# Kernel tuning notes

Measured on AMD Instinct MI355X. Metric: run time of the kernel, lower is better.

The kernel has to match this reference:

```python
import math
import jax, jax.numpy as jnp
import numpy as np

B, S, HID = 2, 1024, 2048
H, D, R = 16, 128, 64            # heads, head_dim, rope_dim_per_head
KVC, QC = 512, 1536              # kv / query compressed dims
MAX_POS = 4096


def _lin(x, w, b):
    return x @ w.T + b


def _rotate_half(x):
    x1, x2 = x[..., : x.shape[-1] // 2], x[..., x.shape[-1] // 2 :]
    return jnp.concatenate([-x2, x1], axis=-1)


def _rope_tables(dim, end, theta=10000.0):
    freqs = 1.0 / (theta ** (jnp.arange(0, dim, 2)[: dim // 2].astype(jnp.float32) / dim))
    f = jnp.outer(jnp.arange(end, dtype=jnp.float32), freqs)  # [end, dim//2]
    cos, sin = jnp.cos(f), jnp.sin(f)
    # duplicate halves so tables broadcast against the full rope dim (standard HF convention)
    return jnp.concatenate([cos, cos], -1), jnp.concatenate([sin, sin], -1)


def setup_inputs() -> dict:
    key = jax.random.key(0)
    ks = jax.random.split(key, 17)
    w = lambda k, shape: (jax.random.normal(k, shape, jnp.float32) * 0.02)
    return {
        "hidden_states": jax.random.normal(ks[0], (B, S, HID), jnp.float32),
        "W_DKV_w": w(ks[1], (KVC, HID)),  "W_DKV_b": w(ks[2], (KVC,)),
        "W_UK_w":  w(ks[3], (H * D, KVC)), "W_UK_b":  w(ks[4], (H * D,)),
        "W_UV_w":  w(ks[5], (H * D, KVC)), "W_UV_b":  w(ks[6], (H * D,)),
        "W_KR_w":  w(ks[7], (R, D)),       "W_KR_b":  w(ks[8], (R,)),
        "W_DQ_w":  w(ks[9], (QC, HID)),    "W_DQ_b":  w(ks[10], (QC,)),
        "W_UQ_w":  w(ks[11], (H * D, QC)), "W_UQ_b":  w(ks[12], (H * D,)),
        "W_QR_w":  w(ks[13], (R, D)),      "W_QR_b":  w(ks[14], (R,)),
        "W_O_w":   w(ks[15], (HID, H * D)),"W_O_b":   w(ks[16], (HID,)),
    }


def reference(hidden_states, W_DKV_w, W_DKV_b, W_UK_w, W_UK_b, W_UV_w, W_UV_b,
              W_KR_w, W_KR_b, W_DQ_w, W_DQ_b, W_UQ_w, W_UQ_b,
              W_QR_w, W_QR_b, W_O_w, W_O_b):
    b, s = hidden_states.shape[:2]
    # latent KV compression + decompression
    c_kv = _lin(hidden_states, W_DKV_w, W_DKV_b)                      # [B,S,KVC]
    k = _lin(c_kv, W_UK_w, W_UK_b).reshape(b, s, H, D)
    v = _lin(c_kv, W_UV_w, W_UV_b).reshape(b, s, H, D)
    # latent Q compression + decompression
    c_q = _lin(hidden_states, W_DQ_w, W_DQ_b)                         # [B,S,QC]
    q = _lin(c_q, W_UQ_w, W_UQ_b).reshape(b, s, H, D)
    # decoupled rope sub-dims
    k_r = _lin(k, W_KR_w, W_KR_b)                                     # [B,S,H,R]
    q_r = _lin(q, W_QR_w, W_QR_b)                                     # [B,S,H,R]
    cos, sin = _rope_tables(R, MAX_POS)
    cos_p = cos[:s][:, None, :]                                       # [S,1,R] -> broadcast over B,H
    sin_p = sin[:s][:, None, :]
    q_r = q_r * cos_p + _rotate_half(q_r) * sin_p
    k_r = k_r * cos_p + _rotate_half(k_r) * sin_p
    # SDPA (no mask, no causal flag in original)
    scale = 1.0 / math.sqrt(D)
    scores = jnp.einsum("bqhd,bkhd->bhqk", q, k) * scale              # [B,H,S,S]
    probs = jax.nn.softmax(scores, axis=-1)
    attn = jnp.einsum("bhqk,bkhd->bqhd", probs, v).reshape(b, s, H * D)
    output = _lin(attn, W_O_w, W_O_b)                                 # [B,S,HID]
    return output, c_kv, k_r
```

## Files before the change

### kernel.cpp

```cpp
#include <hip/hip_runtime.h>
#include <cstdint>

typedef __bf16 bf16;
typedef __attribute__((ext_vector_type(8))) __bf16 bf16x8;
typedef __attribute__((ext_vector_type(4))) float f32x4;

#define MFMA16(a, b, c) __builtin_amdgcn_mfma_f32_16x16x32_bf16(a, b, c, 0, 0, 0)

__device__ __forceinline__ void async16(const bf16* g, bf16* l) {
  __builtin_amdgcn_global_load_lds(
      (const __attribute__((address_space(1))) void*)g,
      (__attribute__((address_space(3))) void*)l, 16, 0, 0);
}

__device__ __forceinline__ bf16x8 load8cvt(const float* p) {
  f32x4 a = *(const f32x4*)p;
  f32x4 b = *(const f32x4*)(p + 4);
  bf16x8 r;
  r[0] = (bf16)a[0]; r[1] = (bf16)a[1]; r[2] = (bf16)a[2]; r[3] = (bf16)a[3];
  r[4] = (bf16)b[0]; r[5] = (bf16)b[1]; r[6] = (bf16)b[2]; r[7] = (bf16)b[3];
  return r;
}

__global__ __launch_bounds__(256) void cvt_f32_bf16(const float* __restrict__ src,
                                                    bf16* __restrict__ dst, int n) {
  int i = (blockIdx.x * 256 + threadIdx.x) * 8;
  if (i >= n) return;
  *(bf16x8*)(dst + i) = load8cvt(src + i);
}

__global__ __launch_bounds__(256) void cvt6(
    const float* __restrict__ s0, bf16* __restrict__ d0, int n0,
    const float* __restrict__ s1, bf16* __restrict__ d1, int n1,
    const float* __restrict__ s2, bf16* __restrict__ d2, int n2,
    const float* __restrict__ s3, bf16* __restrict__ d3, int n3,
    const float* __restrict__ s4, bf16* __restrict__ d4, int n4,
    const float* __restrict__ s5, bf16* __restrict__ d5, int n5) {
  const float* s; bf16* d; int n;
  switch (blockIdx.y) {
    case 0: s = s0; d = d0; n = n0; break;
    case 1: s = s1; d = d1; n = n1; break;
    case 2: s = s2; d = d2; n = n2; break;
    case 3: s = s3; d = d3; n = n3; break;
    case 4: s = s4; d = d4; n = n4; break;
    default: s = s5; d = d5; n = n5; break;
  }
  int i = (blockIdx.x * 256 + threadIdx.x) * 8;
  if (i >= n) return;
  *(bf16x8*)(d + i) = load8cvt(s + i);
}

template <int MODE>
__global__ __launch_bounds__(256) void gemm_bb(
    const bf16* __restrict__ A, int lda,
    const bf16* __restrict__ Bm, int ldb,
    const float* __restrict__ bias0, const float* __restrict__ bias1, int nsplit,
    bf16* __restrict__ outb, float* __restrict__ outf, int ldo,
    int M, int N, int K) {
  __shared__ __align__(16) bf16 As[2][128 * 32];
  __shared__ __align__(16) bf16 Bs[2][64 * 32];
  const int t = threadIdx.x;
  const int lane = t & 63, w = t >> 6;
  const int quad = lane >> 4, l15 = lane & 15;

  const int nwg = gridDim.x * gridDim.y;
  const int id = blockIdx.y * gridDim.x + blockIdx.x;
  const int sw = (id & 7) * (nwg >> 3) + (id >> 3);
  const int bm = (sw / gridDim.x) * 128, bn = (sw % gridDim.x) * 64;

  const int wm = (w >> 1) * 64, wn = (w & 1) * 32;

  f32x4 acc[4][2] = {};

  const int srow = t >> 2;
  const int scol = (t & 3) * 8;
  const bf16* Ap = A + (int64_t)(bm + srow) * lda + scol;
  const bf16* Bp = Bm + (int64_t)(bn + srow) * ldb + scol;

  auto STAGE = [&](int buf, int k0) {
    async16(Ap + k0, &As[buf][w * 512]);
    async16(Ap + (int64_t)64 * lda + k0, &As[buf][2048 + w * 512]);
    async16(Bp + k0, &Bs[buf][w * 512]);
  };
  auto COMPUTE = [&](int buf) {
    bf16x8 a[4], bq[2];
#pragma unroll
    for (int mt = 0; mt < 4; ++mt)
      a[mt] = *(const bf16x8*)(&As[buf][(wm + mt * 16 + l15) * 32 + quad * 8]);
#pragma unroll
    for (int nt = 0; nt < 2; ++nt)
      bq[nt] = *(const bf16x8*)(&Bs[buf][(wn + nt * 16 + l15) * 32 + quad * 8]);
#pragma unroll
    for (int mt = 0; mt < 4; ++mt)
#pragma unroll
      for (int nt = 0; nt < 2; ++nt)
        acc[mt][nt] = MFMA16(a[mt], bq[nt], acc[mt][nt]);
  };

  STAGE(0, 0);
  for (int k0 = 0; k0 < K; k0 += 64) {
    STAGE(1, k0 + 32);
    asm volatile("s_waitcnt vmcnt(3)\n\ts_barrier" ::: "memory");
    COMPUTE(0);
    asm volatile("s_waitcnt lgkmcnt(0)\n\ts_barrier" ::: "memory");
    if (k0 + 64 < K) {
      STAGE(0, k0 + 64);
      asm volatile("s_waitcnt vmcnt(3)\n\ts_barrier" ::: "memory");
    } else {
      asm volatile("s_waitcnt vmcnt(0)\n\ts_barrier" ::: "memory");
    }
    COMPUTE(1);
    asm volatile("s_waitcnt lgkmcnt(0)\n\ts_barrier" ::: "memory");
  }

  float bv[2];
#pragma unroll
  for (int nt = 0; nt < 2; ++nt) {
    int n = bn + wn + nt * 16 + l15;
    bv[nt] = (n < nsplit) ? bias0[n] : bias1[n - nsplit];
  }
#pragma unroll
  for (int mt = 0; mt < 4; ++mt)
#pragma unroll
    for (int nt = 0; nt < 2; ++nt)
#pragma unroll
      for (int r = 0; r < 4; ++r) {
        int64_t m = bm + wm + mt * 16 + quad * 4 + r;
        int n = bn + wn + nt * 16 + l15;
        float v = acc[mt][nt][r] + bv[nt];
        if (MODE != 1) outb[m * ldo + n] = (bf16)v;
        if (MODE == 1) outf[m * (int64_t)ldo + n] = v;
        if (MODE == 2 && n < nsplit) outf[m * nsplit + n] = v;
      }
}

__global__ __launch_bounds__(256) void kr_rope(const bf16* __restrict__ kmat,
                                               const float* __restrict__ Wkr,
                                               const float* __restrict__ bkr,
                                               float* __restrict__ krout) {
  const int t = threadIdx.x;
  const int lane = t & 63, w = t >> 6;
  const int quad = lane >> 4, l15 = lane & 15;
  const int row0 = blockIdx.x * 64 + w * 16;

  const int rr = row0 + l15;
  const bf16* krow = kmat + (int64_t)(rr >> 4) * 4096 + (rr & 15) * 128;
  bf16x8 af[4];
#pragma unroll
  for (int ks = 0; ks < 4; ++ks)
    af[ks] = *(const bf16x8*)(krow + ks * 32 + quad * 8);

  f32x4 acc[4] = {};
#pragma unroll
  for (int nt = 0; nt < 4; ++nt)
#pragma unroll
    for (int ks = 0; ks < 4; ++ks) {
      bf16x8 bf_ = load8cvt(Wkr + (nt * 16 + l15) * 128 + ks * 32 + quad * 8);
      acc[nt] = MFMA16(af[ks], bf_, acc[nt]);
    }

  float bv[4], fr[4];
#pragma unroll
  for (int nt = 0; nt < 4; ++nt) {
    bv[nt] = bkr[nt * 16 + l15];
    int j = ((nt & 1) * 16 + l15);
    fr[nt] = exp2f(-(float)j * 0.41524101186092034f);
  }

#pragma unroll
  for (int r = 0; r < 4; ++r) {
    int row = row0 + quad * 4 + r;
    int pos = (row >> 4) & 1023;
    float val[4];
#pragma unroll
    for (int nt = 0; nt < 4; ++nt) val[nt] = acc[nt][r] + bv[nt];
#pragma unroll
    for (int nt = 0; nt < 4; ++nt) {
      int n = nt * 16 + l15;
      float ang = (float)pos * fr[nt];
      float c = cosf(ang), s = sinf(ang);
      float partner = val[nt ^ 2];
      float o = val[nt] * c + ((nt < 2) ? -partner : partner) * s;
      krout[(int64_t)row * 64 + n] = o;
    }
  }
}

__global__ __launch_bounds__(512, 2) void attn_fwd(const bf16* __restrict__ q,
                                                   const bf16* __restrict__ k,
                                                   const bf16* __restrict__ v,
                                                   bf16* __restrict__ attn) {
  const int bh = blockIdx.x * 4 + (blockIdx.y >> 3);
  const int qt = blockIdx.y & 7;
  const int b = bh >> 4, h = bh & 15;
  __shared__ __align__(16) bf16 Kb[2][64 * 128];
  __shared__ __align__(16) bf16 Vt[128 * 72];
  __shared__ __align__(16) bf16 Pl[8][16 * 72];

  const int t = threadIdx.x;
  const int lane = t & 63, w = t >> 6;
  const int quad = lane >> 4, l15 = lane & 15;
  const int trow = b * 1024 + qt * 128 + w * 16;
  const float scale = 0.08838834764831845f;

  bf16x8 qf[4];
#pragma unroll
  for (int ks = 0; ks < 4; ++ks)
    qf[ks] = *(const bf16x8*)(q + (int64_t)(trow + l15) * 2048 + h * 128 +
                              ks * 32 + quad * 8);

  const bf16* kbase = k + (int64_t)b * 1024 * 4096 + h * 128;
  const int lrow = lane >> 4;
  const int64_t koff0 = (int64_t)(w * 8 + lrow) * 4096 + (((lane & 15) ^ lrow) << 3);
  const int64_t koff1 = (int64_t)(w * 8 + 4 + lrow) * 4096 +
                        (((lane & 15) ^ (4 + lrow)) << 3);

  const int skey = t >> 4;
  const int sd0 = (t & 15) * 8;
  const bf16* vp = v + (int64_t)b * 1024 * 4096 + h * 128 + sd0;

  async16(kbase + koff0, &Kb[0][w * 1024]);
  async16(kbase + koff1, &Kb[0][w * 1024 + 512]);
  bf16x8 vreg[2];
#pragma unroll
  for (int r = 0; r < 2; ++r)
    vreg[r] = *(const bf16x8*)(vp + (int64_t)(r * 32 + skey) * 4096);

  f32x4 o[8] = {};
  float lrw[4] = {0.f, 0.f, 0.f, 0.f};

  for (int kt = 0; kt < 16; ++kt) {
    const int cur = kt & 1;
#pragma unroll
    for (int r = 0; r < 2; ++r) {
      int key = r * 32 + skey;
      int col = (((key >> 3) ^ ((sd0 >> 3) & 7)) << 3) + (key & 7);
#pragma unroll
      for (int j = 0; j < 8; ++j) Vt[(sd0 + j) * 72 + col] = vreg[r][j];
    }
    __syncthreads();

    if (kt + 1 < 16) {
      const bf16* kn = kbase + (int64_t)(kt + 1) * 64 * 4096;
      async16(kn + koff0, &Kb[cur ^ 1][w * 1024]);
      async16(kn + koff1, &Kb[cur ^ 1][w * 1024 + 512]);
#pragma unroll
      for (int r = 0; r < 2; ++r)
        vreg[r] = *(const bf16x8*)(vp + (int64_t)((kt + 1) * 64 + r * 32 + skey) * 4096);
    }

    f32x4 s[4] = {};
    __builtin_amdgcn_s_setprio(1);
#pragma unroll
    for (int nt = 0; nt < 4; ++nt)
#pragma unroll
      for (int ks = 0; ks < 4; ++ks) {
        int key = nt * 16 + l15;
        bf16x8 bfrg = *(const bf16x8*)(
            &Kb[cur][key * 128 + (((ks * 4 + quad) ^ (l15 & 7)) << 3)]);
        s[nt] = MFMA16(qf[ks], bfrg, s[nt]);
      }
    __builtin_amdgcn_s_setprio(0);

    float rsum[4] = {0.f, 0.f, 0.f, 0.f};
#pragma unroll
    for (int nt = 0; nt < 4; ++nt)
#pragma unroll
      for (int r = 0; r < 4; ++r) {
        float p = __expf(s[nt][r] * scale);
        rsum[r] += p;
        int row = quad * 4 + r;
        int blk = (nt * 2 + (l15 >> 3)) ^ (quad * 2 + (r >> 1));
        Pl[w][row * 72 + (blk << 3) + (l15 & 7)] = (bf16)p;
      }
#pragma unroll
    for (int r = 0; r < 4; ++r) lrw[r] += rsum[r];

    __builtin_amdgcn_s_setprio(1);
#pragma unroll
    for (int ks = 0; ks < 2; ++ks) {
      int ablk = (ks * 4 + quad) ^ (l15 >> 1);
      bf16x8 afrg = *(const bf16x8*)(&Pl[w][l15 * 72 + (ablk << 3)]);
#pragma unroll
      for (int dt = 0; dt < 8; ++dt) {
        int d = dt * 16 + l15;
        int kb = ((ks * 4 + quad) ^ ((d >> 3) & 7)) << 3;
        bf16x8 bfrg = *(const bf16x8*)(Vt + d * 72 + kb);
        o[dt] = MFMA16(afrg, bfrg, o[dt]);
      }
    }
    __builtin_amdgcn_s_setprio(0);
    asm volatile("s_waitcnt lgkmcnt(0)\n\ts_barrier" ::: "memory");
  }

  float inv[4];
#pragma unroll
  for (int r = 0; r < 4; ++r) {
    float ssum = lrw[r];
#pragma unroll
    for (int off = 8; off >= 1; off >>= 1) ssum += __shfl_xor(ssum, off, 64);
    inv[r] = 1.0f / ssum;
  }
#pragma unroll
  for (int dt = 0; dt < 8; ++dt)
#pragma unroll
    for (int r = 0; r < 4; ++r) {
      int64_t row = trow + quad * 4 + r;
      int col = h * 128 + dt * 16 + l15;
      attn[row * 2048 + col] = (bf16)(o[dt][r] * inv[r]);
    }
}

extern "C" void kernel_launch(void* const* d_in, const int* in_sizes, int n_in,
                              void* d_out, int out_size, void* d_ws, size_t ws_size,
                              hipStream_t stream) {
  const float* hidden = (const float*)d_in[0];
  const float* Wdkv = (const float*)d_in[1];
  const float* bdkv = (const float*)d_in[2];
  const float* Wuk  = (const float*)d_in[3];
  const float* buk  = (const float*)d_in[4];
  const float* Wuv  = (const float*)d_in[5];
  const float* buv  = (const float*)d_in[6];
  const float* Wkr  = (const float*)d_in[7];
  const float* bkr  = (const float*)d_in[8];
  const float* Wdq  = (const float*)d_in[9];
  const float* bdq  = (const float*)d_in[10];
  const float* Wuq  = (const float*)d_in[11];
  const float* buq  = (const float*)d_in[12];
  const float* Wo   = (const float*)d_in[15];
  const float* bo   = (const float*)d_in[16];

  float* out0 = (float*)d_out;
  float* c_kv = out0 + 4194304;
  float* k_r  = out0 + 5242880;

  bf16* DKVQ = (bf16*)d_ws;
  bf16* KV   = DKVQ + 4194304;

  bf16* WT   = KV;
  bf16* qx   = (bf16*)out0;
  bf16* hb   = qx + 4194304;
  bf16* WUKV = qx;
  bf16* Wuqb = hb;
  bf16* Wob  = (bf16*)k_r;

  cvt6<<<dim3(2048, 6), 256, 0, stream>>>(
      hidden, hb, 4194304,
      Wdkv, WT, 1048576,
      Wdq, WT + 1048576, 3145728,
      Wuk, WUKV, 1048576,
      Wuv, WUKV + 1048576, 1048576,
      Wo, Wob, 4194304);
  gemm_bb<2><<<dim3(32, 16), 256, 0, stream>>>(hb, 2048, WT, 2048, bdkv, bdq, 512,
                                               DKVQ, c_kv, 2048, 2048, 2048, 2048);
  cvt_f32_bf16<<<1536, 256, 0, stream>>>(Wuq, Wuqb, 3145728);
  gemm_bb<0><<<dim3(64, 16), 256, 0, stream>>>(DKVQ, 2048, WUKV, 512, buk, buv, 2048,
                                               KV, nullptr, 4096, 2048, 4096, 512);
  gemm_bb<0><<<dim3(32, 16), 256, 0, stream>>>(DKVQ + 512, 2048, Wuqb, 1536, buq, buq,
                                               2048, qx, nullptr, 2048, 2048, 2048, 1536);
  attn_fwd<<<dim3(8, 32), 512, 0, stream>>>(qx, KV, KV + 2048, DKVQ);
  gemm_bb<1><<<dim3(32, 16), 256, 0, stream>>>(DKVQ, 2048, Wob, 2048, bo, bo, 2048,
                                               nullptr, out0, 2048, 2048, 2048, 2048);
  kr_rope<<<512, 256, 0, stream>>>(KV, Wkr, bkr, k_r);
}
```

Baseline: 312.1 us.

## Deepen GEMM prefetch to four stages and halve attention block size

The GEMM mainloop moves from a two-buffer ping-pong to a four-slot ring buffer with three K-slices in flight, and the vmcnt waits are adjusted so the tail drains correctly. This is meant to hide more global-load latency, at the cost of doubling LDS use per block. The attention kernel drops from 512 to 256 threads per block (64 query rows instead of 128) and uses twice as many blocks, so each thread now loads four K/V rows per tile. This raises block count for better CU fill but means each K/V tile is reloaded by twice as many blocks.

```diff
diff --git a/kernel.cpp b/kernel.cpp
--- a/kernel.cpp
+++ b/kernel.cpp
@@ -57,8 +57,8 @@
     const float* __restrict__ bias0, const float* __restrict__ bias1, int nsplit,
     bf16* __restrict__ outb, float* __restrict__ outf, int ldo,
     int M, int N, int K) {
-  __shared__ __align__(16) bf16 As[2][128 * 32];
-  __shared__ __align__(16) bf16 Bs[2][64 * 32];
+  __shared__ __align__(16) bf16 As[4][128 * 32];
+  __shared__ __align__(16) bf16 Bs[4][64 * 32];
   const int t = threadIdx.x;
   const int lane = t & 63, w = t >> 6;
   const int quad = lane >> 4, l15 = lane & 15;
@@ -97,19 +97,21 @@
         acc[mt][nt] = MFMA16(a[mt], bq[nt], acc[mt][nt]);
   };
 
+  const int K32 = K >> 5;
   STAGE(0, 0);
-  for (int k0 = 0; k0 < K; k0 += 64) {
-    STAGE(1, k0 + 32);
-    asm volatile("s_waitcnt vmcnt(3)\n\ts_barrier" ::: "memory");
-    COMPUTE(0);
-    asm volatile("s_waitcnt lgkmcnt(0)\n\ts_barrier" ::: "memory");
-    if (k0 + 64 < K) {
-      STAGE(0, k0 + 64);
-      asm volatile("s_waitcnt vmcnt(3)\n\ts_barrier" ::: "memory");
+  STAGE(1, 32);
+  STAGE(2, 64);
+  for (int s = 0; s < K32; ++s) {
+    if (s + 3 < K32) {
+      STAGE((s + 3) & 3, (s + 3) << 5);
+      asm volatile("s_waitcnt vmcnt(9)\n\ts_barrier" ::: "memory");
     } else {
-      asm volatile("s_waitcnt vmcnt(0)\n\ts_barrier" ::: "memory");
-    }
-    COMPUTE(1);
+      const int rem = K32 - 1 - s;
+      if (rem >= 2)      asm volatile("s_waitcnt vmcnt(6)\n\ts_barrier" ::: "memory");
+      else if (rem == 1) asm volatile("s_waitcnt vmcnt(3)\n\ts_barrier" ::: "memory");
+      else               asm volatile("s_waitcnt vmcnt(0)\n\ts_barrier" ::: "memory");
+    }
+    COMPUTE(s & 3);
     asm volatile("s_waitcnt lgkmcnt(0)\n\ts_barrier" ::: "memory");
   }
 
@@ -186,21 +188,21 @@
   }
 }
 
-__global__ __launch_bounds__(512, 2) void attn_fwd(const bf16* __restrict__ q,
+__global__ __launch_bounds__(256, 2) void attn_fwd(const bf16* __restrict__ q,
                                                    const bf16* __restrict__ k,
                                                    const bf16* __restrict__ v,
                                                    bf16* __restrict__ attn) {
-  const int bh = blockIdx.x * 4 + (blockIdx.y >> 3);
-  const int qt = blockIdx.y & 7;
+  const int bh = blockIdx.x * 4 + (blockIdx.y >> 4);
+  const int qt = blockIdx.y & 15;
   const int b = bh >> 4, h = bh & 15;
   __shared__ __align__(16) bf16 Kb[2][64 * 128];
   __shared__ __align__(16) bf16 Vt[128 * 72];
-  __shared__ __align__(16) bf16 Pl[8][16 * 72];
+  __shared__ __align__(16) bf16 Pl[4][16 * 72];
 
   const int t = threadIdx.x;
   const int lane = t & 63, w = t >> 6;
   const int quad = lane >> 4, l15 = lane & 15;
-  const int trow = b * 1024 + qt * 128 + w * 16;
+  const int trow = b * 1024 + qt * 64 + w * 16;
   const float scale = 0.08838834764831845f;
 
   bf16x8 qf[4];
@@ -211,20 +213,24 @@
 
   const bf16* kbase = k + (int64_t)b * 1024 * 4096 + h * 128;
   const int lrow = lane >> 4;
-  const int64_t koff0 = (int64_t)(w * 8 + lrow) * 4096 + (((lane & 15) ^ lrow) << 3);
-  const int64_t koff1 = (int64_t)(w * 8 + 4 + lrow) * 4096 +
-                        (((lane & 15) ^ (4 + lrow)) << 3);
+  int64_t koff[4];
+#pragma unroll
+  for (int c = 0; c < 4; ++c) {
+    int row = w * 16 + c * 4 + lrow;
+    koff[c] = (int64_t)row * 4096 + (((lane & 15) ^ (row & 7)) << 3);
+  }
 
   const int skey = t >> 4;
   const int sd0 = (t & 15) * 8;
   const bf16* vp = v + (int64_t)b * 1024 * 4096 + h * 128 + sd0;
 
-  async16(kbase + koff0, &Kb[0][w * 1024]);
-  async16(kbase + koff1, &Kb[0][w * 1024 + 512]);
-  bf16x8 vreg[2];
-#pragma unroll
-  for (int r = 0; r < 2; ++r)
-    vreg[r] = *(const bf16x8*)(vp + (int64_t)(r * 32 + skey) * 4096);
+#pragma unroll
+  for (int c = 0; c < 4; ++c)
+    async16(kbase + koff[c], &Kb[0][w * 2048 + c * 512]);
+  bf16x8 vreg[4];
+#pragma unroll
+  for (int r = 0; r < 4; ++r)
+    vreg[r] = *(const bf16x8*)(vp + (int64_t)(r * 16 + skey) * 4096);
 
   f32x4 o[8] = {};
   float lrw[4] = {0.f, 0.f, 0.f, 0.f};
@@ -232,8 +238,8 @@
   for (int kt = 0; kt < 16; ++kt) {
     const int cur = kt & 1;
 #pragma unroll
-    for (int r = 0; r < 2; ++r) {
-      int key = r * 32 + skey;
+    for (int r = 0; r < 4; ++r) {
+      int key = r * 16 + skey;
       int col = (((key >> 3) ^ ((sd0 >> 3) & 7)) << 3) + (key & 7);
 #pragma unroll
       for (int j = 0; j < 8; ++j) Vt[(sd0 + j) * 72 + col] = vreg[r][j];
@@ -242,11 +248,12 @@
 
     if (kt + 1 < 16) {
       const bf16* kn = kbase + (int64_t)(kt + 1) * 64 * 4096;
-      async16(kn + koff0, &Kb[cur ^ 1][w * 1024]);
-      async16(kn + koff1, &Kb[cur ^ 1][w * 1024 + 512]);
-#pragma unroll
-      for (int r = 0; r < 2; ++r)
-        vreg[r] = *(const bf16x8*)(vp + (int64_t)((kt + 1) * 64 + r * 32 + skey) * 4096);
+#pragma unroll
+      for (int c = 0; c < 4; ++c)
+        async16(kn + koff[c], &Kb[cur ^ 1][w * 2048 + c * 512]);
+#pragma unroll
+      for (int r = 0; r < 4; ++r)
+        vreg[r] = *(const bf16x8*)(vp + (int64_t)((kt + 1) * 64 + r * 16 + skey) * 4096);
     }
 
     f32x4 s[4] = {};
@@ -358,7 +365,7 @@
                                                KV, nullptr, 4096, 2048, 4096, 512);
   gemm_bb<0><<<dim3(32, 16), 256, 0, stream>>>(DKVQ + 512, 2048, Wuqb, 1536, buq, buq,
                                                2048, qx, nullptr, 2048, 2048, 2048, 1536);
-  attn_fwd<<<dim3(8, 32), 512, 0, stream>>>(qx, KV, KV + 2048, DKVQ);
+  attn_fwd<<<dim3(8, 64), 256, 0, stream>>>(qx, KV, KV + 2048, DKVQ);
   gemm_bb<1><<<dim3(32, 16), 256, 0, stream>>>(DKVQ, 2048, Wob, 2048, bo, bo, 2048,
                                                nullptr, out0, 2048, 2048, 2048, 2048);
   kr_rope<<<512, 256, 0, stream>>>(KV, Wkr, bkr, k_r);
```

Measured after the change: 323.3 us. +3.6%, slower.
